# Optimization experiments

Hardware: AMD Instinct MI355X
Metric: run time of the kernel (lower is better)

The kernel has to match this reference:

```python
import jax, jax.numpy as jnp
import numpy as np

B, NUM_OBJECTS, NUM_ATTRS, T = 8, 128, 4, 12
MAX_CONCEPTS, EMBED_DIM, IDENTITY_DIM, ATTENTION_DIM, HIDDEN_DIM = 2048, 128, 64, 64, 256
OP_MODE, OP_INSERT, OP_TRANSFER = 0, 1, 2


def setup_inputs() -> dict:
    key = jax.random.key(0)
    ks = jax.random.split(key, 24)
    def rn(k, shape, s=0.05):
        return s * jax.random.normal(k, shape, dtype=jnp.float32)
    return {
        'scene': jax.random.randint(ks[0], (B, NUM_OBJECTS, NUM_ATTRS), 0, MAX_CONCEPTS - 1),
        'program_op': jax.random.randint(ks[1], (B, T), 0, 3),
        'program_arg': jax.random.randint(ks[2], (B, T), 0, MAX_CONCEPTS),
        'attr_emb_in': rn(ks[3], (MAX_CONCEPTS, EMBED_DIM)),
        'attr_emb_out': rn(ks[4], (MAX_CONCEPTS, EMBED_DIM)),
        'attr_emb_id': rn(ks[5], (MAX_CONCEPTS, IDENTITY_DIM)),
        'concept_emb_in': rn(ks[6], (MAX_CONCEPTS, EMBED_DIM)),
        'concept_emb_out': rn(ks[7], (MAX_CONCEPTS, EMBED_DIM)),
        'concept_emb_id': rn(ks[8], (MAX_CONCEPTS, IDENTITY_DIM)),
        'embed_init': rn(ks[9], (EMBED_DIM,)),
        'identity_init': rn(ks[10], (IDENTITY_DIM,)),
        'attention_init': jnp.zeros((ATTENTION_DIM,), dtype=jnp.float32),
        'axon_w1': rn(ks[11], (HIDDEN_DIM, ATTENTION_DIM + IDENTITY_DIM)),
        'axon_b1': rn(ks[12], (HIDDEN_DIM,)),
        'axon_w2': rn(ks[13], (ATTENTION_DIM, HIDDEN_DIM)),
        'axon_b2': rn(ks[14], (ATTENTION_DIM,)),
        'meta_w1': rn(ks[15], (HIDDEN_DIM, EMBED_DIM + ATTENTION_DIM)),
        'meta_b1': rn(ks[16], (HIDDEN_DIM,)),
        'meta_w2': rn(ks[17], (ATTENTION_DIM, HIDDEN_DIM)),
        'meta_b2': rn(ks[18], (ATTENTION_DIM,)),
    }


def _mlp(x, w1, b1, w2, b2):
    # torch Linear convention: y = x @ W.T + b
    return jnp.maximum(x @ w1.T + b1, 0.0) @ w2.T + b2


def reference(scene, program_op, program_arg, attr_emb_in, attr_emb_out, attr_emb_id,
              concept_emb_in, concept_emb_out, concept_emb_id,
              embed_init, identity_init, attention_init,
              axon_w1, axon_b1, axon_w2, axon_b2,
              meta_w1, meta_b1, meta_w2, meta_b2):
    Bq, N, _ = scene.shape
    C = MAX_CONCEPTS + N  # dim_concept
    mask = (scene != -1).astype(jnp.float32)  # (B,N,A) non-background mask
    def embed_bg(E):
        return (E[scene + 1] * mask[..., None]).sum(2)  # (B,N,D)
    objects_in = embed_bg(attr_emb_in)
    objects_out = embed_bg(attr_emb_out)
    objects_id = embed_bg(attr_emb_id)

    rep = lambda w: jnp.broadcast_to(w[None], (Bq,) + w.shape)
    dendron = jnp.concatenate([rep(concept_emb_in), objects_in], 1)    # (B,C,E)
    axon = jnp.concatenate([rep(concept_emb_out), objects_out], 1)     # (B,C,E)
    identity = jnp.concatenate([rep(concept_emb_id), objects_id], 1)   # (B,C,Id)
    weight_matrix = jnp.einsum('bie,bje->bij', dendron, axon)           # (B,C,C)

    arguments = concept_emb_out[program_arg]                            # (B,T,E)
    is_mode = (program_op == OP_MODE).astype(jnp.float32)               # (B,T)
    is_insert = (program_op == OP_INSERT).astype(jnp.float32)
    is_transfer = (program_op == OP_TRANSFER).astype(jnp.float32)

    meta0 = jnp.broadcast_to(attention_init[None], (Bq, ATTENTION_DIM))
    att0 = jnp.broadcast_to(attention_init[None, None], (Bq, C, ATTENTION_DIM))

    def step(carry, xs):
        meta, attention = carry
        arg_i, m, ins, tr = xs  # (B,E), (B,), (B,), (B,)
        new_meta = _mlp(jnp.concatenate([meta, arg_i], 1), meta_w1, meta_b1, meta_w2, meta_b2)
        meta = m[:, None] * new_meta + (1.0 - m[:, None]) * meta
        # (arguments * axon).mean over embed dim -> (B,C)
        proj = jnp.einsum('be,bce->bc', arg_i, axon) / EMBED_DIM
        attention_insert = meta[:, None, :] * proj[:, :, None]          # (B,C,A)
        attended_weight = weight_matrix * attention.mean(2)[:, None, :] # (B,C,C)
        ia = jnp.concatenate([identity, attention], 2)                  # (B,C,Id+A)
        # (attended_weight[:,:,:,None] * ia[:,None]).mean(2) == matmul / C
        gathered = jnp.einsum('bij,bjd->bid', attended_weight, ia) / C  # (B,C,Id+A)
        attention_transfer = _mlp(gathered, axon_w1, axon_b1, axon_w2, axon_b2) + gathered[..., IDENTITY_DIM:]
        attention = attention + ins[:, None, None] * attention_insert + tr[:, None, None] * attention_transfer
        attention = jnp.clip(jnp.where(attention >= 0, attention, 0.01 * attention), -1.0, 2.0)
        return (meta, attention), (attention, attention_insert, attention_transfer)

    xs = (jnp.swapaxes(arguments, 0, 1), is_mode.T, is_insert.T, is_transfer.T)
    (meta, attention), (att_hist, ins_hist, trans_hist) = jax.lax.scan(step, (meta0, att0), xs)
    output_softmax = jax.nn.log_softmax(attention.mean(2), axis=1)  # (B,C)
    return (output_softmax, att_hist, ins_hist, trans_hist)
```

## Files before the change

kernel.cpp:

```cpp
#include <hip/hip_runtime.h>

#define B 8
#define NOBJ 128
#define NATTR 4
#define T 12
#define MC 2048
#define E 128
#define IDD 64
#define AD 64
#define HD 256
#define C 2176

typedef short s16x8 __attribute__((ext_vector_type(8)));
typedef float f32x4 __attribute__((ext_vector_type(4)));

__device__ inline unsigned short f2b(float f) {
  union { float f; unsigned u; } v; v.f = f;
  unsigned r = v.u + 0x7FFFu + ((v.u >> 16) & 1u);
  return (unsigned short)(r >> 16);
}
__device__ inline float b2f(unsigned short u) {
  union { unsigned u; float f; } v; v.u = ((unsigned)u) << 16;
  return v.f;
}

__device__ __forceinline__ void st_coh_u64(unsigned long long* p, unsigned long long v) {
  __hip_atomic_store(p, v, __ATOMIC_RELAXED, __HIP_MEMORY_SCOPE_AGENT);
}
__device__ __forceinline__ void st_coh_u32(unsigned* p, unsigned v) {
  __hip_atomic_store(p, v, __ATOMIC_RELAXED, __HIP_MEMORY_SCOPE_AGENT);
}
__device__ __forceinline__ void st_coh_f32(float* p, float v) {
  union { float f; unsigned u; } c; c.f = v;
  __hip_atomic_store((unsigned*)p, c.u, __ATOMIC_RELAXED, __HIP_MEMORY_SCOPE_AGENT);
}
__device__ __forceinline__ unsigned ld_coh_u32(const unsigned* p) {
  return __hip_atomic_load(p, __ATOMIC_RELAXED, __HIP_MEMORY_SCOPE_AGENT);
}

__device__ __forceinline__ int gidx(int r, int c) {
  return r * 128 + ((((c >> 3) ^ (r & 15)) << 3) | (c & 7));
}
__device__ __forceinline__ int hidx(int r, int c) {
  return r * 256 + ((((c >> 3) ^ (r & 15)) << 3) | (c & 7));
}
__device__ __forceinline__ int mtidx(int r, int c) {
  return r * 128 + ((((c >> 3) ^ (r & 15)) << 3) | (c & 7));
}

__global__ __launch_bounds__(256) void k_setupA(
    const int* __restrict__ scene,
    const float* __restrict__ aein,
    const float* __restrict__ cein,
    const float* __restrict__ aw1, const float* __restrict__ aw2,
    const float* __restrict__ mw1, const float* __restrict__ mw2,
    unsigned short* __restrict__ dendron_bf,
    unsigned short* __restrict__ w1_bf, unsigned short* __restrict__ w2_bf,
    float* __restrict__ mw1T, float* __restrict__ mw2T,
    unsigned* __restrict__ flags) {
  int blk = blockIdx.x;
  int tid = threadIdx.x;
  if (blk < 4352) {
    int gid = blk * 2 + (tid >> 7);
    int e = tid & 127;
    int b = gid / C, j = gid % C;
    float din;
    if (j < MC) {
      din = cein[j * E + e];
    } else {
      int obj = j - MC;
      float sIn = 0.f;
      for (int a = 0; a < NATTR; a++) {
        int s = scene[(b * NOBJ + obj) * NATTR + a];
        float m = (s != -1) ? 1.f : 0.f;
        sIn += aein[(s + 1) * E + e] * m;
      }
      din = sIn;
    }
    dendron_bf[(size_t)gid * E + e] = f2b(din);
  } else if (blk < 4544) {
    int i = (blk - 4352) * 256 + tid;
    if (i < HD * E)  w1_bf[i] = f2b(aw1[i]);
    if (i < AD * HD) w2_bf[i] = f2b(aw2[i]);
    if (i < 192 * HD) { int c = i / HD, k = i % HD; mw1T[c * HD + k] = mw1[k * 192 + c]; }
    if (i < HD * AD)  { int k = i / AD, a = i % AD; mw2T[k * AD + a] = mw2[a * HD + k]; }
  } else {
    for (int i = tid; i < 512; i += 256) flags[i] = 0u;
  }
}

__global__ __launch_bounds__(256) void k_setupB(
    const int* __restrict__ scene,
    const float* __restrict__ aeout, const float* __restrict__ aeid,
    const float* __restrict__ ceout, const float* __restrict__ ceid,
    const float* __restrict__ att_init,
    const int* __restrict__ prog_op, const int* __restrict__ prog_arg,
    const float* __restrict__ mw1T, const float* __restrict__ mb1,
    const float* __restrict__ mw2T, const float* __restrict__ mb2,
    unsigned short* __restrict__ axonT, unsigned short* __restrict__ idT_g,
    unsigned short* __restrict__ siaT, float* __restrict__ att_g,
    float* __restrict__ meta_all, float* __restrict__ proj_all) {
  int blk = blockIdx.x;
  int tid = threadIdx.x;
  __shared__ float sbuf[13952];
  if (blk < 272) {
    int b = blk / 34, jc = blk % 34;
    int j0 = jc * 64;
    float* ax   = sbuf;
    float* idb  = sbuf + 64 * 129;
    float* argL = idb + 64 * 65;
    int lane = tid & 63, lr = lane & 15;
    float s = att_init[lane];
    s += __shfl_xor(s, 1, 64);  s += __shfl_xor(s, 2, 64);
    s += __shfl_xor(s, 4, 64);  s += __shfl_xor(s, 8, 64);
    s += __shfl_xor(s, 16, 64); s += __shfl_xor(s, 32, 64);
    float am0 = s * (1.f / AD);
    for (int i = tid; i < 64 * 128; i += 256) {
      int j = i >> 7, e = i & 127;
      int jg = j0 + j;
      float v;
      if (jg < MC) v = ceout[jg * E + e];
      else {
        int obj = jg - MC;
        v = 0.f;
        for (int a = 0; a < NATTR; a++) {
          int sc = scene[(b * NOBJ + obj) * NATTR + a];
          float m = (sc != -1) ? 1.f : 0.f;
          v += aeout[(sc + 1) * E + e] * m;
        }
      }
      ax[j * 129 + e] = v;
    }
    for (int i = tid; i < 64 * 64; i += 256) {
      int j = i >> 6, d = i & 63;
      int jg = j0 + j;
      float v;
      if (jg < MC) v = ceid[jg * IDD + d];
      else {
        int obj = jg - MC;
        v = 0.f;
        for (int a = 0; a < NATTR; a++) {
          int sc = scene[(b * NOBJ + obj) * NATTR + a];
          float m = (sc != -1) ? 1.f : 0.f;
          v += aeid[(sc + 1) * IDD + d] * m;
        }
      }
      idb[j * 65 + d] = v;
    }
    for (int i = tid; i < T * 128; i += 256) {
      int t = i >> 7, e = i & 127;
      int arg = prog_arg[b * T + t];
      argL[t * 128 + e] = ceout[arg * E + e];
    }
    __syncthreads();
    for (int i = tid; i < 128 * 64; i += 256) {
      int e = i >> 6, jj = i & 63;
      axonT[(size_t)(b * E + e) * C + j0 + jj] = f2b(ax[jj * 129 + e]);
    }
    for (int i = tid; i < 64 * 64; i += 256) {
      int d = i >> 6, jj = i & 63;
      idT_g[(size_t)(b * 64 + d) * C + j0 + jj] = f2b(idb[jj * 65 + d]);
      siaT[(size_t)(b * 128 + d) * C + j0 + jj] = f2b(idb[jj * 65 + d] * am0);
      siaT[(size_t)(b * 128 + 64 + d) * C + j0 + jj] = f2b(att_init[d] * am0);
    }
    {
      float* ag = att_g + (size_t)blk * 4096 + tid * 16;
      #pragma unroll
      for (int n = 0; n < 4; n++) {
        float v0 = att_init[n * 16 + lr];
        #pragma unroll
        for (int v = 0; v < 4; v++) ag[n * 4 + v] = v0;
      }
    }
    {
      int jj = tid & 63, tq = tid >> 6;
      #pragma unroll
      for (int sI = 0; sI < 3; sI++) {
        int t = tq + 4 * sI;
        const float* ar = argL + t * 128;
        const float* axr = ax + jj * 129;
        float acc = 0.f;
        #pragma unroll 8
        for (int e = 0; e < 128; e++) acc += axr[e] * ar[e];
        proj_all[((size_t)t * B + b) * C + j0 + jj] = acc * (1.f / E);
      }
    }
  } else {
    int b = blk - 272;
    float* x = sbuf;
    float* h = sbuf + 192;
    float* meta = h + 256;
    if (tid < AD) meta[tid] = att_init[tid];
    __syncthreads();
    for (int t = 0; t < T; t++) {
      int arg = prog_arg[b * T + t];
      if (tid < AD) x[tid] = meta[tid];
      else if (tid < 192) x[tid] = ceout[arg * E + (tid - 64)];
      __syncthreads();
      float s = mb1[tid];
      for (int c = 0; c < 192; c++) s += x[c] * mw1T[c * HD + tid];
      h[tid] = fmaxf(s, 0.f);
      __syncthreads();
      if (tid < AD) {
        float o = mb2[tid];
        for (int k = 0; k < HD; k++) o += h[k] * mw2T[k * AD + tid];
        float m = (prog_op[b * T + t] == 0) ? 1.f : 0.f;
        float nm = m * o + (1.f - m) * meta[tid];
        meta[tid] = nm;
        meta_all[(t * B + b) * AD + tid] = nm;
      }
      __syncthreads();
    }
  }
}

__global__ __launch_bounds__(256) void k_step(
    int t,
    const unsigned short* __restrict__ dendron_bf,
    const unsigned short* __restrict__ axonT,
    const unsigned short* __restrict__ idT_g,
    const unsigned short* __restrict__ siaT_in,
    const unsigned short* __restrict__ w1_bf, const float* __restrict__ b1g,
    const unsigned short* __restrict__ w2_bf, const float* __restrict__ b2g,
    const float* __restrict__ proj_all, const float* __restrict__ meta_all,
    const int* __restrict__ prog_op,
    unsigned long long* __restrict__ Mt64,
    float* __restrict__ att_g, unsigned short* __restrict__ siaT_out,
    float* __restrict__ rowmean, float* __restrict__ out,
    float* __restrict__ att_hist, float* __restrict__ ins_hist,
    float* __restrict__ trans_hist,
    unsigned* __restrict__ mflag, unsigned* __restrict__ sflag) {
  const int blk = blockIdx.x;
  const int b = blk / 34, ch = blk % 34, j0 = ch * 64;
  const int tid = threadIdx.x;
  const int w = tid >> 6, lane = tid & 63, lr = lane & 15, lg = lane >> 4;

  __shared__ unsigned short smem[24576];
  __shared__ float am_l[64];
  __shared__ float red[256];
  unsigned short* g_l = smem;
  unsigned short* mt  = smem + 8192;
  unsigned short* h_l = smem + 8192;
  float* mred = (float*)smem;

  const f32x4 z = {0.f, 0.f, 0.f, 0.f};
  const unsigned ph = (unsigned)(t + 1);

  float att[4][4];
  {
    const f32x4* ag = (const f32x4*)(att_g + (size_t)blk * 4096 + tid * 16);
    #pragma unroll
    for (int n = 0; n < 4; n++) {
      f32x4 v4 = ag[n];
      #pragma unroll
      for (int v = 0; v < 4; v++) att[n][v] = v4[v];
    }
  }

  if (ch < 16) {
    int d0 = (ch >> 2) * 32, e0 = (ch & 3) * 32;
    const unsigned short* ap0 = siaT_in + (size_t)(b * 128 + d0 + lr) * C + w * 544 + lg * 8;
    const unsigned short* ap1 = ap0 + (size_t)16 * C;
    const unsigned short* bp0 = axonT + (size_t)(b * E + e0 + lr) * C + w * 544 + lg * 8;
    const unsigned short* bp1 = bp0 + (size_t)16 * C;
    f32x4 a00 = z, a01 = z, a10 = z, a11 = z;
    #pragma unroll 4
    for (int kk = 0; kk < 17; kk++) {
      int k0 = kk * 32;
      s16x8 A0 = *(const s16x8*)(ap0 + k0);
      s16x8 A1 = *(const s16x8*)(ap1 + k0);
      s16x8 B0 = *(const s16x8*)(bp0 + k0);
      s16x8 B1 = *(const s16x8*)(bp1 + k0);
      a00 = __builtin_amdgcn_mfma_f32_16x16x32_bf16(A0, B0, a00, 0, 0, 0);
      a01 = __builtin_amdgcn_mfma_f32_16x16x32_bf16(A0, B1, a01, 0, 0, 0);
      a10 = __builtin_amdgcn_mfma_f32_16x16x32_bf16(A1, B0, a10, 0, 0, 0);
      a11 = __builtin_amdgcn_mfma_f32_16x16x32_bf16(A1, B1, a11, 0, 0, 0);
    }
    #pragma unroll
    for (int v = 0; v < 4; v++) {
      mred[(w * 32 + lg * 4 + v) * 33 + lr]           = a00[v];
      mred[(w * 32 + lg * 4 + v) * 33 + 16 + lr]      = a01[v];
      mred[(w * 32 + 16 + lg * 4 + v) * 33 + lr]      = a10[v];
      mred[(w * 32 + 16 + lg * 4 + v) * 33 + 16 + lr] = a11[v];
    }
    __syncthreads();
    {
      int r = tid >> 3, c = (tid & 7) * 4;
      float s0 = 0.f, s1 = 0.f, s2 = 0.f, s3 = 0.f;
      #pragma unroll
      for (int w4 = 0; w4 < 4; w4++) {
        const float* p = &mred[(w4 * 32 + r) * 33 + c];
        s0 += p[0]; s1 += p[1]; s2 += p[2]; s3 += p[3];
      }
      unsigned long long pk = (unsigned long long)f2b(s0)
                            | ((unsigned long long)f2b(s1) << 16)
                            | ((unsigned long long)f2b(s2) << 32)
                            | ((unsigned long long)f2b(s3) << 48);
      st_coh_u64(Mt64 + (((size_t)(b * 128 + d0 + r) * 128) + e0 + c) / 4, pk);
    }
    asm volatile("s_waitcnt vmcnt(0)" ::: "memory");
    __syncthreads();
    if (tid == 0) st_coh_u32(mflag + b * 16 + ch, ph);
  }
  if (tid < 16) {
    while (ld_coh_u32(mflag + b * 16 + tid) < ph) __builtin_amdgcn_s_sleep(1);
  }
  __syncthreads();
  {
    const unsigned long long* mtp = Mt64 + (size_t)b * 4096;
    #pragma unroll
    for (int k = 0; k < 16; k++) {
      int idx = tid + k * 256;
      unsigned long long v = mtp[idx];
      int r = idx >> 5, c4 = (idx & 31) * 4;
      *(unsigned long long*)&mt[mtidx(r, c4)] = v;
    }
  }
  __syncthreads();
  {
    s16x8 afr[4];
    #pragma unroll
    for (int ke = 0; ke < 4; ke++)
      afr[ke] = *(const s16x8*)(dendron_bf + (size_t)(b * C + j0 + w * 16 + lr) * E + ke * 32 + lg * 8);
    #pragma unroll
    for (int n = 0; n < 8; n++) {
      f32x4 acc = z;
      #pragma unroll
      for (int ke = 0; ke < 4; ke++) {
        s16x8 bf = *(const s16x8*)&mt[mtidx(n * 16 + lr, ke * 32 + lg * 8)];
        acc = __builtin_amdgcn_mfma_f32_16x16x32_bf16(afr[ke], bf, acc, 0, 0, 0);
      }
      #pragma unroll
      for (int v = 0; v < 4; v++)
        g_l[gidx(w * 16 + lg * 4 + v, n * 16 + lr)] = f2b(acc[v] * (1.f / C));
    }
  }
  __syncthreads();
  {
    s16x8 gf[4];
    #pragma unroll
    for (int kd = 0; kd < 4; kd++)
      gf[kd] = *(const s16x8*)&g_l[gidx(w * 16 + lr, kd * 32 + lg * 8)];
    #pragma unroll
    for (int n = 0; n < 16; n++) {
      f32x4 acc = z;
      #pragma unroll
      for (int kd = 0; kd < 4; kd++) {
        s16x8 bf = *(const s16x8*)(w1_bf + (size_t)(n * 16 + lr) * E + kd * 32 + lg * 8);
        acc = __builtin_amdgcn_mfma_f32_16x16x32_bf16(gf[kd], bf, acc, 0, 0, 0);
      }
      float b1v = b1g[n * 16 + lr];
      #pragma unroll
      for (int v = 0; v < 4; v++)
        h_l[hidx(w * 16 + lg * 4 + v, n * 16 + lr)] = f2b(fmaxf(acc[v] + b1v, 0.f));
    }
  }
  __syncthreads();
  {
    s16x8 hf[8];
    #pragma unroll
    for (int kk = 0; kk < 8; kk++)
      hf[kk] = *(const s16x8*)&h_l[hidx(w * 16 + lr, kk * 32 + lg * 8)];
    int op = prog_op[b * T + t];
    float insF = (op == 1) ? 1.f : 0.f, trF = (op == 2) ? 1.f : 0.f;
    float projv[4];
    #pragma unroll
    for (int v = 0; v < 4; v++)
      projv[v] = proj_all[(size_t)(t * B + b) * C + j0 + w * 16 + lg * 4 + v];
    #pragma unroll
    for (int n = 0; n < 4; n++) {
      f32x4 acc = z;
      #pragma unroll
      for (int kk = 0; kk < 8; kk++) {
        s16x8 bf = *(const s16x8*)(w2_bf + (size_t)(n * 16 + lr) * HD + kk * 32 + lg * 8);
        acc = __builtin_amdgcn_mfma_f32_16x16x32_bf16(hf[kk], bf, acc, 0, 0, 0);
      }
      int a = n * 16 + lr;
      float b2v = b2g[a];
      float meta_a = meta_all[(size_t)(t * B + b) * AD + a];
      #pragma unroll
      for (int v = 0; v < 4; v++) {
        int row = lg * 4 + v;
        int i = j0 + w * 16 + row;
        float transfer = acc[v] + b2v + b2f(g_l[gidx(w * 16 + row, 64 + a)]);
        float insert = meta_a * projv[v];
        float attv = att[n][v] + insF * insert + trF * transfer;
        attv = (attv >= 0.f) ? attv : 0.01f * attv;
        attv = fminf(fmaxf(attv, -1.f), 2.f);
        att[n][v] = attv;
        size_t hi = (((size_t)t * B + b) * C + i) * AD + a;
        __builtin_nontemporal_store(attv, att_hist + hi);
        __builtin_nontemporal_store(insert, ins_hist + hi);
        __builtin_nontemporal_store(transfer, trans_hist + hi);
      }
    }
  }
  float amr[4];
  {
    float s[4];
    #pragma unroll
    for (int v = 0; v < 4; v++) s[v] = att[0][v] + att[1][v] + att[2][v] + att[3][v];
    #pragma unroll
    for (int v = 0; v < 4; v++) {
      s[v] += __shfl_xor(s[v], 1, 64);
      s[v] += __shfl_xor(s[v], 2, 64);
      s[v] += __shfl_xor(s[v], 4, 64);
      s[v] += __shfl_xor(s[v], 8, 64);
      amr[v] = s[v] * (1.f / AD);
    }
    if (lr == 0) {
      #pragma unroll
      for (int v = 0; v < 4; v++) am_l[w * 16 + lg * 4 + v] = amr[v];
    }
  }
  if (t < T - 1) {
    {
      f32x4* ag = (f32x4*)(att_g + (size_t)blk * 4096 + tid * 16);
      #pragma unroll
      for (int n = 0; n < 4; n++) {
        f32x4 v4;
        #pragma unroll
        for (int v = 0; v < 4; v++) v4[v] = att[n][v];
        ag[n] = v4;
        unsigned long long pk = 0;
        #pragma unroll
        for (int v = 0; v < 4; v++)
          pk |= (unsigned long long)f2b(att[n][v] * amr[v]) << (16 * v);
        *(unsigned long long*)(siaT_out + (size_t)(b * 128 + 64 + n * 16 + lr) * C + j0 + w * 16 + lg * 4) = pk;
      }
    }
    __syncthreads();
    #pragma unroll
    for (int k2 = 0; k2 < 2; k2++) {
      int idx = tid + k2 * 256;
      int d = idx >> 3, part = idx & 7;
      int j = part * 8;
      s16x8 iv = *(const s16x8*)(idT_g + (size_t)(b * 64 + d) * C + j0 + j);
      s16x8 ov;
      #pragma unroll
      for (int m = 0; m < 8; m++)
        ov[m] = (short)f2b(b2f((unsigned short)iv[m]) * am_l[j + m]);
      *(s16x8*)(siaT_out + (size_t)(b * 128 + d) * C + j0 + j) = ov;
    }
  } else {
    if (lr == 0) {
      #pragma unroll
      for (int v = 0; v < 4; v++)
        st_coh_f32(rowmean + (size_t)b * C + j0 + w * 16 + lg * 4 + v, amr[v]);
    }
    asm volatile("s_waitcnt vmcnt(0)" ::: "memory");
    __syncthreads();
    if (tid == 0) st_coh_u32(sflag + b * 34 + ch, 1u);
    if (ch == 0) {
      if (tid < 34) {
        while (ld_coh_u32(sflag + b * 34 + tid) < 1u) __builtin_amdgcn_s_sleep(1);
      }
      __syncthreads();
      float* am = (float*)smem;
      for (int i = tid; i < C; i += 256) am[i] = rowmean[(size_t)b * C + i];
      __syncthreads();
      float mx = -1e30f;
      for (int i = tid; i < C; i += 256) mx = fmaxf(mx, am[i]);
      red[tid] = mx; __syncthreads();
      for (int s2 = 128; s2 > 0; s2 >>= 1) { if (tid < s2) red[tid] = fmaxf(red[tid], red[tid + s2]); __syncthreads(); }
      mx = red[0]; __syncthreads();
      float sm = 0.f;
      for (int i = tid; i < C; i += 256) sm += expf(am[i] - mx);
      red[tid] = sm; __syncthreads();
      for (int s2 = 128; s2 > 0; s2 >>= 1) { if (tid < s2) red[tid] += red[tid + s2]; __syncthreads(); }
      float lse = logf(red[0]) + mx;
      for (int i = tid; i < C; i += 256) out[(size_t)b * C + i] = am[i] - lse;
    }
  }
}

extern "C" void kernel_launch(void* const* d_in, const int* in_sizes, int n_in,
                              void* d_out, int out_size, void* d_ws, size_t ws_size,
                              hipStream_t stream) {
  const int* scene     = (const int*)d_in[0];
  const int* prog_op   = (const int*)d_in[1];
  const int* prog_arg  = (const int*)d_in[2];
  const float* aein    = (const float*)d_in[3];
  const float* aeout   = (const float*)d_in[4];
  const float* aeid    = (const float*)d_in[5];
  const float* cein    = (const float*)d_in[6];
  const float* ceout   = (const float*)d_in[7];
  const float* ceid    = (const float*)d_in[8];
  const float* att_init = (const float*)d_in[11];
  const float* aw1 = (const float*)d_in[12];
  const float* ab1 = (const float*)d_in[13];
  const float* aw2 = (const float*)d_in[14];
  const float* ab2 = (const float*)d_in[15];
  const float* mw1 = (const float*)d_in[16];
  const float* mb1 = (const float*)d_in[17];
  const float* mw2 = (const float*)d_in[18];
  const float* mb2 = (const float*)d_in[19];

  char* ws = (char*)d_ws;
  size_t off = 0;
  auto carve = [&](size_t bytes) { char* p = ws + off; off += (bytes + 255) & ~(size_t)255; return p; };
  float* proj_all  = (float*)carve((size_t)T * B * C * 4);
  float* meta_all  = (float*)carve((size_t)T * B * AD * 4);
  float* mw1T      = (float*)carve((size_t)192 * HD * 4);
  float* mw2T      = (float*)carve((size_t)HD * AD * 4);
  float* rowmean   = (float*)carve((size_t)B * C * 4);
  float* att_g     = (float*)carve((size_t)272 * 4096 * 4);
  unsigned short* dendron_bf = (unsigned short*)carve((size_t)B * C * E * 2);
  unsigned short* axonT      = (unsigned short*)carve((size_t)B * E * C * 2);
  unsigned short* idT_g      = (unsigned short*)carve((size_t)B * 64 * C * 2);
  unsigned short* siaT       = (unsigned short*)carve((size_t)B * 128 * C * 2);
  unsigned long long* Mt64   = (unsigned long long*)carve((size_t)B * 4096 * 8);
  unsigned short* w1_bf      = (unsigned short*)carve((size_t)HD * E * 2);
  unsigned short* w2_bf      = (unsigned short*)carve((size_t)AD * HD * 2);
  unsigned*       flags      = (unsigned*)carve(2048);
  unsigned*       mflag = flags;
  unsigned*       sflag = flags + 128;

  float* out_sm     = (float*)d_out;
  float* att_hist   = out_sm + B * C;
  float* ins_hist   = att_hist + (size_t)T * B * C * AD;
  float* trans_hist = ins_hist + (size_t)T * B * C * AD;

  k_setupA<<<dim3(4545), dim3(256), 0, stream>>>(scene, aein, cein, aw1, aw2, mw1, mw2,
                                                 dendron_bf, w1_bf, w2_bf, mw1T, mw2T, flags);
  k_setupB<<<dim3(280), dim3(256), 0, stream>>>(scene, aeout, aeid, ceout, ceid, att_init,
                                                prog_op, prog_arg, mw1T, mb1, mw2T, mb2,
                                                axonT, idT_g, siaT, att_g,
                                                meta_all, proj_all);
  for (int t = 0; t < T; t++) {
    k_step<<<dim3(272), dim3(256), 0, stream>>>(t, dendron_bf, axonT, idT_g, siaT,
                                                w1_bf, ab1, w2_bf, ab2,
                                                proj_all, meta_all, prog_op,
                                                Mt64, att_g, siaT, rowmean, out_sm,
                                                att_hist, ins_hist, trans_hist,
                                                mflag, sflag);
  }
}
```

Measured before the change: 648.1 us.

## Compute per-chunk partial M products in previous step instead of re-reading siaT

```diff
diff --git a/kernel.cpp b/kernel.cpp
--- a/kernel.cpp
+++ b/kernel.cpp
@@ -46,6 +46,9 @@
 }
 __device__ __forceinline__ int mtidx(int r, int c) {
   return r * 128 + ((((c >> 3) ^ (r & 15)) << 3) | (c & 7));
+}
+__device__ __forceinline__ int sidx(int d, int j) {
+  return d * 64 + ((((j >> 3) ^ (d & 7)) << 3) | (j & 7));
 }
 
 __global__ __launch_bounds__(256) void k_setupA(
@@ -225,7 +228,8 @@
     const float* __restrict__ proj_all, const float* __restrict__ meta_all,
     const int* __restrict__ prog_op,
     unsigned long long* __restrict__ Mt64,
-    float* __restrict__ att_g, unsigned short* __restrict__ siaT_out,
+    unsigned short* __restrict__ Mpart,
+    float* __restrict__ att_g,
     float* __restrict__ rowmean, float* __restrict__ out,
     float* __restrict__ att_hist, float* __restrict__ ins_hist,
     float* __restrict__ trans_hist,
@@ -241,6 +245,7 @@
   unsigned short* g_l = smem;
   unsigned short* mt  = smem + 8192;
   unsigned short* h_l = smem + 8192;
+  unsigned short* sia = smem;
   float* mred = (float*)smem;
 
   const f32x4 z = {0.f, 0.f, 0.f, 0.f};
@@ -259,47 +264,69 @@
 
   if (ch < 16) {
     int d0 = (ch >> 2) * 32, e0 = (ch & 3) * 32;
-    const unsigned short* ap0 = siaT_in + (size_t)(b * 128 + d0 + lr) * C + w * 544 + lg * 8;
-    const unsigned short* ap1 = ap0 + (size_t)16 * C;
-    const unsigned short* bp0 = axonT + (size_t)(b * E + e0 + lr) * C + w * 544 + lg * 8;
-    const unsigned short* bp1 = bp0 + (size_t)16 * C;
-    f32x4 a00 = z, a01 = z, a10 = z, a11 = z;
-    #pragma unroll 4
-    for (int kk = 0; kk < 17; kk++) {
-      int k0 = kk * 32;
-      s16x8 A0 = *(const s16x8*)(ap0 + k0);
-      s16x8 A1 = *(const s16x8*)(ap1 + k0);
-      s16x8 B0 = *(const s16x8*)(bp0 + k0);
-      s16x8 B1 = *(const s16x8*)(bp1 + k0);
-      a00 = __builtin_amdgcn_mfma_f32_16x16x32_bf16(A0, B0, a00, 0, 0, 0);
-      a01 = __builtin_amdgcn_mfma_f32_16x16x32_bf16(A0, B1, a01, 0, 0, 0);
-      a10 = __builtin_amdgcn_mfma_f32_16x16x32_bf16(A1, B0, a10, 0, 0, 0);
-      a11 = __builtin_amdgcn_mfma_f32_16x16x32_bf16(A1, B1, a11, 0, 0, 0);
-    }
-    #pragma unroll
-    for (int v = 0; v < 4; v++) {
-      mred[(w * 32 + lg * 4 + v) * 33 + lr]           = a00[v];
-      mred[(w * 32 + lg * 4 + v) * 33 + 16 + lr]      = a01[v];
-      mred[(w * 32 + 16 + lg * 4 + v) * 33 + lr]      = a10[v];
-      mred[(w * 32 + 16 + lg * 4 + v) * 33 + 16 + lr] = a11[v];
-    }
-    __syncthreads();
-    {
+    if (t == 0) {
+      const unsigned short* ap0 = siaT_in + (size_t)(b * 128 + d0 + lr) * C + w * 544 + lg * 8;
+      const unsigned short* ap1 = ap0 + (size_t)16 * C;
+      const unsigned short* bp0 = axonT + (size_t)(b * E + e0 + lr) * C + w * 544 + lg * 8;
+      const unsigned short* bp1 = bp0 + (size_t)16 * C;
+      f32x4 a00 = z, a01 = z, a10 = z, a11 = z;
+      #pragma unroll 4
+      for (int kk = 0; kk < 17; kk++) {
+        int k0 = kk * 32;
+        s16x8 A0 = *(const s16x8*)(ap0 + k0);
+        s16x8 A1 = *(const s16x8*)(ap1 + k0);
+        s16x8 B0 = *(const s16x8*)(bp0 + k0);
+        s16x8 B1 = *(const s16x8*)(bp1 + k0);
+        a00 = __builtin_amdgcn_mfma_f32_16x16x32_bf16(A0, B0, a00, 0, 0, 0);
+        a01 = __builtin_amdgcn_mfma_f32_16x16x32_bf16(A0, B1, a01, 0, 0, 0);
+        a10 = __builtin_amdgcn_mfma_f32_16x16x32_bf16(A1, B0, a10, 0, 0, 0);
+        a11 = __builtin_amdgcn_mfma_f32_16x16x32_bf16(A1, B1, a11, 0, 0, 0);
+      }
+      #pragma unroll
+      for (int v = 0; v < 4; v++) {
+        mred[(w * 32 + lg * 4 + v) * 33 + lr]           = a00[v];
+        mred[(w * 32 + lg * 4 + v) * 33 + 16 + lr]      = a01[v];
+        mred[(w * 32 + 16 + lg * 4 + v) * 33 + lr]      = a10[v];
+        mred[(w * 32 + 16 + lg * 4 + v) * 33 + 16 + lr] = a11[v];
+      }
+      __syncthreads();
+      {
+        int r = tid >> 3, c = (tid & 7) * 4;
+        float s0 = 0.f, s1 = 0.f, s2 = 0.f, s3 = 0.f;
+        #pragma unroll
+        for (int w4 = 0; w4 < 4; w4++) {
+          const float* p = &mred[(w4 * 32 + r) * 33 + c];
+          s0 += p[0]; s1 += p[1]; s2 += p[2]; s3 += p[3];
+        }
+        unsigned long long pk = (unsigned long long)f2b(s0)
+                              | ((unsigned long long)f2b(s1) << 16)
+                              | ((unsigned long long)f2b(s2) << 32)
+                              | ((unsigned long long)f2b(s3) << 48);
+        st_coh_u64(Mt64 + (((size_t)(b * 128 + d0 + r) * 128) + e0 + c) / 4, pk);
+      }
+      asm volatile("s_waitcnt vmcnt(0)" ::: "memory");
+      __syncthreads();
+    } else {
       int r = tid >> 3, c = (tid & 7) * 4;
+      size_t eoff = (size_t)(d0 + r) * 128 + e0 + c;
+      const unsigned long long* pb = (const unsigned long long*)Mpart + ((size_t)b * 34 * 16384 + eoff) / 4;
       float s0 = 0.f, s1 = 0.f, s2 = 0.f, s3 = 0.f;
-      #pragma unroll
-      for (int w4 = 0; w4 < 4; w4++) {
-        const float* p = &mred[(w4 * 32 + r) * 33 + c];
-        s0 += p[0]; s1 += p[1]; s2 += p[2]; s3 += p[3];
+      #pragma unroll 2
+      for (int c2 = 0; c2 < 34; c2++) {
+        unsigned long long u = pb[(size_t)c2 * 4096];
+        s0 += b2f((unsigned short)(u));
+        s1 += b2f((unsigned short)(u >> 16));
+        s2 += b2f((unsigned short)(u >> 32));
+        s3 += b2f((unsigned short)(u >> 48));
       }
       unsigned long long pk = (unsigned long long)f2b(s0)
                             | ((unsigned long long)f2b(s1) << 16)
                             | ((unsigned long long)f2b(s2) << 32)
                             | ((unsigned long long)f2b(s3) << 48);
       st_coh_u64(Mt64 + (((size_t)(b * 128 + d0 + r) * 128) + e0 + c) / 4, pk);
-    }
-    asm volatile("s_waitcnt vmcnt(0)" ::: "memory");
-    __syncthreads();
+      asm volatile("s_waitcnt vmcnt(0)" ::: "memory");
+      __syncthreads();
+    }
     if (tid == 0) st_coh_u32(mflag + b * 16 + ch, ph);
   }
   if (tid < 16) {
@@ -422,25 +449,44 @@
         #pragma unroll
         for (int v = 0; v < 4; v++) v4[v] = att[n][v];
         ag[n] = v4;
-        unsigned long long pk = 0;
+      }
+    }
+    __syncthreads();
+    for (int i = tid; i < 64 * 64; i += 256) {
+      int d = i >> 6, j = i & 63;
+      sia[sidx(d, j)] = f2b(b2f(idT_g[(size_t)(b * 64 + d) * C + j0 + j]) * am_l[j]);
+    }
+    #pragma unroll
+    for (int n = 0; n < 4; n++)
+      #pragma unroll
+      for (int v = 0; v < 4; v++)
+        sia[sidx(64 + n * 16 + lr, w * 16 + lg * 4 + v)] = f2b(att[n][v] * amr[v]);
+    __syncthreads();
+    {
+      s16x8 af[2][2];
+      #pragma unroll
+      for (int dt = 0; dt < 2; dt++) {
+        int d0 = (w * 2 + dt) * 16;
+        af[dt][0] = *(const s16x8*)&sia[sidx(d0 + lr, lg * 8)];
+        af[dt][1] = *(const s16x8*)&sia[sidx(d0 + lr, 32 + lg * 8)];
+      }
+      unsigned short* mp = Mpart + (size_t)blk * 16384;
+      #pragma unroll
+      for (int et = 0; et < 8; et++) {
+        const unsigned short* bp = axonT + (size_t)(b * E + et * 16 + lr) * C + j0 + lg * 8;
+        s16x8 b0 = *(const s16x8*)bp;
+        s16x8 b1 = *(const s16x8*)(bp + 32);
         #pragma unroll
-        for (int v = 0; v < 4; v++)
-          pk |= (unsigned long long)f2b(att[n][v] * amr[v]) << (16 * v);
-        *(unsigned long long*)(siaT_out + (size_t)(b * 128 + 64 + n * 16 + lr) * C + j0 + w * 16 + lg * 4) = pk;
-      }
-    }
-    __syncthreads();
-    #pragma unroll
-    for (int k2 = 0; k2 < 2; k2++) {
-      int idx = tid + k2 * 256;
-      int d = idx >> 3, part = idx & 7;
-      int j = part * 8;
-      s16x8 iv = *(const s16x8*)(idT_g + (size_t)(b * 64 + d) * C + j0 + j);
-      s16x8 ov;
-      #pragma unroll
-      for (int m = 0; m < 8; m++)
-        ov[m] = (short)f2b(b2f((unsigned short)iv[m]) * am_l[j + m]);
-      *(s16x8*)(siaT_out + (size_t)(b * 128 + d) * C + j0 + j) = ov;
+        for (int dt = 0; dt < 2; dt++) {
+          f32x4 acc = z;
+          acc = __builtin_amdgcn_mfma_f32_16x16x32_bf16(af[dt][0], b0, acc, 0, 0, 0);
+          acc = __builtin_amdgcn_mfma_f32_16x16x32_bf16(af[dt][1], b1, acc, 0, 0, 0);
+          int d0 = (w * 2 + dt) * 16;
+          #pragma unroll
+          for (int v = 0; v < 4; v++)
+            mp[(d0 + lg * 4 + v) * 128 + et * 16 + lr] = f2b(acc[v]);
+        }
+      }
     }
   } else {
     if (lr == 0) {
@@ -510,6 +556,7 @@
   unsigned short* idT_g      = (unsigned short*)carve((size_t)B * 64 * C * 2);
   unsigned short* siaT       = (unsigned short*)carve((size_t)B * 128 * C * 2);
   unsigned long long* Mt64   = (unsigned long long*)carve((size_t)B * 4096 * 8);
+  unsigned short* Mpart      = (unsigned short*)carve((size_t)272 * 16384 * 2);
   unsigned short* w1_bf      = (unsigned short*)carve((size_t)HD * E * 2);
   unsigned short* w2_bf      = (unsigned short*)carve((size_t)AD * HD * 2);
   unsigned*       flags      = (unsigned*)carve(2048);
@@ -531,7 +578,7 @@
     k_step<<<dim3(272), dim3(256), 0, stream>>>(t, dendron_bf, axonT, idT_g, siaT,
                                                 w1_bf, ab1, w2_bf, ab2,
                                                 proj_all, meta_all, prog_op,
-                                                Mt64, att_g, siaT, rowmean, out_sm,
+                                                Mt64, Mpart, att_g, rowmean, out_sm,
                                                 att_hist, ins_hist, trans_hist,
                                                 mflag, sflag);
   }
```

Measured after the change: 680.4 us. +5.0%, slower.
